# Kernel optimization log

Measured on AMD Instinct MI355X. Metric: run time of the kernel, lower is better.

## Reference

```python
import jax, jax.numpy as jnp
import numpy as np

NE, NR, D, H, L = 200000, 500, 128, 4, 2
HD = D // H
N, E, B = 32768, 262144, 256
MARGIN = 1.0


def setup_inputs() -> dict:
    key = jax.random.key(0)
    ks = jax.random.split(key, 16)
    nrm = lambda k, shp, s=0.05: jax.random.normal(k, shp, jnp.float32) * s
    inp = {
        'ent_emb': nrm(ks[0], (NE, D)),
        'rel_emb': nrm(ks[1], (NR, D)),
        'rel_prior': nrm(ks[2], (NR, 1)),
    }
    for i, nm in enumerate(['Wq', 'Wk', 'Wv', 'Wo', 'Wek', 'Wev']):
        inp[nm] = nrm(ks[3 + i], (L, D, D))
    for gi, g in enumerate(['h', 't', 'n']):
        kb = jax.random.fold_in(key, 100 + gi)
        k1, k2, k3, k4 = jax.random.split(kb, 4)
        inp[f'x_{g}'] = jax.random.randint(k1, (N,), 0, NE, jnp.int32)
        inp[f'ei_{g}'] = jax.random.randint(k2, (2, E), 0, N, jnp.int32)
        inp[f'ea_{g}'] = jax.random.randint(k3, (E,), 0, NR, jnp.int32)
        inp[f'y_{g}'] = jax.random.randint(k4, (B,), 0, N // B, jnp.int32)
        inp[f's_{g}'] = jnp.full((B,), N // B, dtype=jnp.int32)
    inp['sample'] = jax.random.randint(ks[9], (B, 3), 0, NR, jnp.int32)
    return inp


def gnn_embed(ent_emb, rel_emb, rel_prior, Wq, Wk, Wv, Wo, Wek, Wev, x, ei, ea, y, s):
    n = x.shape[0]
    h = ent_emb[x]                    # [N, D] node features (embedding lookup)
    e_emb = rel_emb[ea]               # [E, D] edge relation embedding
    e_pri = rel_prior[ea]             # [E, 1] scalar relation prior gate
    src, dst = ei[0], ei[1]
    scale = 1.0 / np.sqrt(HD).astype(np.float32)
    for l in range(L):
        q = (h @ Wq[l]).reshape(n, H, HD)[dst]                               # [E,H,HD]
        k = (h @ Wk[l]).reshape(n, H, HD)[src] + (e_emb @ Wek[l]).reshape(-1, H, HD)
        v = (h @ Wv[l]).reshape(n, H, HD)[src] + (e_emb @ Wev[l]).reshape(-1, H, HD)
        score = jnp.sum(q * k, axis=-1) * scale * e_pri                      # [E,H]
        # segment softmax over incoming edges of each destination node
        m = jax.ops.segment_max(score, dst, num_segments=n)
        m = jnp.where(jnp.isfinite(m), m, 0.0)
        ex = jnp.exp(score - m[dst])
        den = jax.ops.segment_sum(ex, dst, num_segments=n)[dst]
        alpha = ex / (den + 1e-16)                                           # [E,H]
        msg = jax.ops.segment_sum((alpha[..., None] * v).reshape(-1, D), dst, num_segments=n)
        h = jax.nn.gelu(h + msg @ Wo[l])                                     # residual + activation
    # get_real_index: exclusive cumsum of graph sizes + local target index
    offsets = jnp.concatenate([jnp.zeros((1,), s.dtype), jnp.cumsum(s)[:-1]])
    return h[offsets + y]             # [B, D]


def reference(ent_emb, rel_emb, rel_prior, Wq, Wk, Wv, Wo, Wek, Wev,
              x_h, ei_h, ea_h, y_h, s_h,
              x_t, ei_t, ea_t, y_t, s_t,
              x_n, ei_n, ea_n, y_n, s_n, sample):
    g = lambda x, ei, ea, y, s: gnn_embed(ent_emb, rel_emb, rel_prior, Wq, Wk, Wv, Wo, Wek, Wev, x, ei, ea, y, s)
    h = g(x_h, ei_h, ea_h, y_h, s_h)[:, None, :]   # [B,1,D]
    t = g(x_t, ei_t, ea_t, y_t, s_t)[:, None, :]
    tn = g(x_n, ei_n, ea_n, y_n, s_n)[:, None, :]
    r = rel_emb[sample[:, 1]][:, None, :]          # [B,1,D]
    proj_t = h + r                                 # TransE projection
    pos = jnp.linalg.norm(t - proj_t + 1e-8, axis=2)   # [B,1]
    negs = jnp.linalg.norm(t - tn + 1e-8, axis=2)      # [B,1]
    neg = jnp.mean(negs, axis=-1)                      # [B]
    # MarginRankingLoss(pos, neg, target=-1): mean(max(0, (pos-neg)+margin)); broadcasts [B,1]-[B] -> [B,B]
    loss = jnp.mean(jnp.maximum(pos - neg + MARGIN, 0.0))
    return loss
```

## Files before the change

### kernel.cpp

```cpp
#include <hip/hip_runtime.h>
#include <hip/hip_bf16.h>
#include <math.h>

#define NEC 200000
#define NRC 500
#define DD 128
#define LLC 2
#define NNODE 32768
#define EEDGE 262144
#define BBATCH 256
#define NG 3
#define BCAP 32

typedef __attribute__((ext_vector_type(8))) short short8;
typedef __attribute__((ext_vector_type(4))) float floatx4;
typedef __attribute__((ext_vector_type(2))) float floatx2;

__device__ __forceinline__ float bf2f(unsigned short u) {
  union { unsigned int i; float f; } c; c.i = ((unsigned int)u) << 16; return c.f;
}
__device__ __forceinline__ unsigned short f2bf(float f) {
  union { float f; unsigned int i; } c; c.f = f;
  unsigned int x = c.i;
  unsigned int r = x + 0x7fffu + ((x >> 16) & 1u);
  return (unsigned short)(r >> 16);
}
__device__ __forceinline__ float bfu_lo(unsigned int u) {
  union { unsigned int i; float f; } c; c.i = u << 16; return c.f;
}
__device__ __forceinline__ float bfu_hi(unsigned int u) {
  union { unsigned int i; float f; } c; c.i = u & 0xffff0000u; return c.f;
}

__device__ __forceinline__ bool detect_fm(const void* ent) {
  unsigned int u = ((const unsigned int*)ent)[threadIdx.x & 63];
  bool big = fabsf(bfu_lo(u)) > 100.f;
  return __ballot(big) != 0ull;
}

__global__ __launch_bounds__(128) void k_prep(const void* ent, const void* rel,
    const void* prior, const void* Wq, const void* Wk, const void* Wv, const void* Wo,
    const void* Wek, const void* Wev,
    float* pris, unsigned short* WT, unsigned short* relk, unsigned short* relv, int* deg) {
  bool fm = detect_fm(ent);
  int bid = blockIdx.x, tid = threadIdx.x;
  if (bid < 4) {
    int r = bid * 128 + tid;
    if (r < NRC) {
      float p = fm ? ((const float*)prior)[r] : bf2f(((const unsigned short*)prior)[r]);
      pris[r] = p * 0.17677669529663687f;
    }
  } else if (bid < 1028) {
    int t = (bid - 4) * 128 + tid;
    int mat = t >> 15;
    int rem = t & 32767;
    int l = rem >> 14;
    int p = rem & 16383;
    int d = p >> 7, c = p & 127;
    const void* W = mat == 0 ? Wq : (mat == 1 ? Wk : (mat == 2 ? Wv : Wo));
    size_t src = (size_t)l * DD * DD + (size_t)c * DD + d;
    float v = fm ? ((const float*)W)[src] : bf2f(((const unsigned short*)W)[src]);
    WT[(((size_t)mat * LLC + l) * DD + d) * DD + c] = f2bf(v);
  } else if (bid < 3028) {
    int rid = bid - 1028;
    int which = rid / 1000;
    int l = (rid / 500) % 2;
    int r = rid % 500;
    int d = tid;
    size_t wofs = (size_t)l * DD * DD;
    const float* Wf = (const float*)(which ? Wev : Wek) + wofs;
    const unsigned short* Wb = (const unsigned short*)(which ? Wev : Wek) + wofs;
    __shared__ float re[DD];
    re[d] = fm ? ((const float*)rel)[r * DD + d] : bf2f(((const unsigned short*)rel)[r * DD + d]);
    __syncthreads();
    float acc = 0.f;
    if (fm) { for (int c = 0; c < DD; ++c) acc += re[c] * Wf[c * DD + d]; }
    else    { for (int c = 0; c < DD; ++c) acc += re[c] * bf2f(Wb[c * DD + d]); }
    unsigned short* out = which ? relv : relk;
    out[((size_t)l * NRC + r) * DD + d] = f2bf(acc);
  } else {
    int t = (bid - 3028) * 128 + tid;
    uint4 z = {0u, 0u, 0u, 0u};
    ((uint4*)deg)[t * 2] = z;
    ((uint4*)deg)[t * 2 + 1] = z;
  }
}

__global__ __launch_bounds__(256) void k_gb(const void* ent,
    const int* x0, const int* x1, const int* x2,
    const int* ei0, const int* ea0, const int* ei1, const int* ea1,
    const int* ei2, const int* ea2,
    unsigned short* hbf, int* deg, unsigned int* bucket) {
  int bid = blockIdx.x, tid = threadIdx.x;
  if (bid < 3072) {
    bool fm = detect_fm(ent);
    int rbase = bid * 32;
    int g = rbase >> 15;
    const int* x = g == 0 ? x0 : (g == 1 ? x1 : x2);
    int c = tid & 31;
    int j4 = tid >> 5;
    int rows[4], xs[4];
    #pragma unroll
    for (int k = 0; k < 4; ++k) {
      rows[k] = rbase + j4 + 8 * k;
      xs[k] = x[rows[k] & (NNODE - 1)];
    }
    if (fm) {
      float4 v[4];
      #pragma unroll
      for (int k = 0; k < 4; ++k)
        v[k] = *reinterpret_cast<const float4*>((const float*)ent + (size_t)xs[k] * DD + c * 4);
      #pragma unroll
      for (int k = 0; k < 4; ++k) {
        uint2 o;
        o.x = ((unsigned int)f2bf(v[k].y) << 16) | (unsigned int)f2bf(v[k].x);
        o.y = ((unsigned int)f2bf(v[k].w) << 16) | (unsigned int)f2bf(v[k].z);
        *reinterpret_cast<uint2*>(hbf + (size_t)rows[k] * DD + c * 4) = o;
      }
    } else {
      uint2 v[4];
      #pragma unroll
      for (int k = 0; k < 4; ++k)
        v[k] = *reinterpret_cast<const uint2*>((const unsigned short*)ent + (size_t)xs[k] * DD + c * 4);
      #pragma unroll
      for (int k = 0; k < 4; ++k)
        *reinterpret_cast<uint2*>(hbf + (size_t)rows[k] * DD + c * 4) = v[k];
    }
  } else {
    int bb = bid - 3072;
    int g = bb >> 10;
    const int* ei = g == 0 ? ei0 : (g == 1 ? ei1 : ei2);
    const int* ea = g == 0 ? ea0 : (g == 1 ? ea1 : ea2);
    int e = (bb & 1023) * 256 + tid;
    int dst = ei[EEDGE + e];
    int src = ei[e];
    int r = ea[e];
    int pos = atomicAdd(&deg[g * NNODE + dst], 1);
    if (pos < BCAP)
      bucket[((size_t)g * NNODE + dst) * BCAP + pos] = (unsigned int)src | ((unsigned int)r << 15);
  }
}

__device__ __forceinline__ void stage_wt(const unsigned short* WT, int tid,
                                         unsigned short (*Wt)[136]) {
  #pragma unroll
  for (int pass = 0; pass < 8; ++pass) {
    int idx = pass * 256 + tid;
    int d = idx >> 4, c0 = (idx & 15) << 3;
    *reinterpret_cast<short8*>(&Wt[d][c0]) =
        *reinterpret_cast<const short8*>(WT + d * DD + c0);
  }
}

__global__ __launch_bounds__(256) void k_gemm_qkv(const unsigned short* A,
    const unsigned short* WT, int layer, unsigned short* Qo, unsigned char* KV) {
  __shared__ unsigned short Wt[DD][136];
  int mat = blockIdx.y;
  int g = blockIdx.z;
  const unsigned short* Ag = A + (size_t)g * NNODE * DD;
  int tid = threadIdx.x;
  stage_wt(WT + ((size_t)mat * LLC + layer) * DD * DD, tid, Wt);
  __syncthreads();
  int w = tid >> 6, lane = tid & 63;
  int m = lane & 15, quad = lane >> 4;
  int row = blockIdx.x * 64 + w * 16 + m;
  floatx4 acc[8];
  #pragma unroll
  for (int t = 0; t < 8; ++t) acc[t] = (floatx4){0.f, 0.f, 0.f, 0.f};
  const unsigned short* arow = Ag + (size_t)row * DD;
  #pragma unroll
  for (int ks = 0; ks < 4; ++ks) {
    short8 a = *reinterpret_cast<const short8*>(arow + ks * 32 + quad * 8);
    #pragma unroll
    for (int t = 0; t < 8; ++t) {
      short8 b = *reinterpret_cast<const short8*>(&Wt[t * 16 + m][ks * 32 + quad * 8]);
      acc[t] = __builtin_amdgcn_mfma_f32_16x16x32_bf16(a, b, acc[t], 0, 0, 0);
    }
  }
  __syncthreads();
  unsigned short* ut = &Wt[0][0];
  #pragma unroll
  for (int t = 0; t < 8; ++t) {
    #pragma unroll
    for (int r = 0; r < 4; ++r) {
      ut[(w * 16 + quad * 4 + r) * 136 + t * 16 + m] = f2bf(acc[t][r]);
    }
  }
  __syncthreads();
  int rowbase = blockIdx.x * 64;
  if (mat == 0) {
    unsigned short* Og = Qo + (size_t)g * NNODE * DD;
    #pragma unroll
    for (int k = 0; k < 4; ++k) {
      int flat = k * 256 + tid;
      int rw = flat >> 4, c8 = flat & 15;
      short8 v = *reinterpret_cast<const short8*>(ut + rw * 136 + c8 * 8);
      *reinterpret_cast<short8*>(Og + (size_t)(rowbase + rw) * DD + c8 * 8) = v;
    }
  } else {
    unsigned char* kvb = KV + (size_t)g * NNODE * 256 + (mat == 1 ? 0 : 128);
    #pragma unroll
    for (int k = 0; k < 2; ++k) {
      int flat = k * 256 + tid;
      int rw = flat >> 3, c16 = flat & 7;
      const unsigned short* p = ut + rw * 136 + c16 * 16;
      uint4 a = *reinterpret_cast<const uint4*>(p);
      uint4 b = *reinterpret_cast<const uint4*>(p + 8);
      unsigned int w0 = __builtin_amdgcn_cvt_pk_fp8_f32(bfu_lo(a.x), bfu_hi(a.x), 0u, false);
      w0 = __builtin_amdgcn_cvt_pk_fp8_f32(bfu_lo(a.y), bfu_hi(a.y), w0, true);
      unsigned int w1 = __builtin_amdgcn_cvt_pk_fp8_f32(bfu_lo(a.z), bfu_hi(a.z), 0u, false);
      w1 = __builtin_amdgcn_cvt_pk_fp8_f32(bfu_lo(a.w), bfu_hi(a.w), w1, true);
      unsigned int w2 = __builtin_amdgcn_cvt_pk_fp8_f32(bfu_lo(b.x), bfu_hi(b.x), 0u, false);
      w2 = __builtin_amdgcn_cvt_pk_fp8_f32(bfu_lo(b.y), bfu_hi(b.y), w2, true);
      unsigned int w3 = __builtin_amdgcn_cvt_pk_fp8_f32(bfu_lo(b.z), bfu_hi(b.z), 0u, false);
      w3 = __builtin_amdgcn_cvt_pk_fp8_f32(bfu_lo(b.w), bfu_hi(b.w), w3, true);
      uint4 o = {w0, w1, w2, w3};
      *reinterpret_cast<uint4*>(kvb + (size_t)(rowbase + rw) * 256 + c16 * 16) = o;
    }
  }
}

__global__ __launch_bounds__(256) void k_gemm_o(const unsigned short* A,
    const unsigned short* WT, int layer, unsigned short* hbf) {
  __shared__ unsigned short Wt[DD][136];
  int g = blockIdx.y;
  const unsigned short* Ag = A + (size_t)g * NNODE * DD;
  unsigned short* hbg = hbf + (size_t)g * NNODE * DD;
  int tid = threadIdx.x;
  stage_wt(WT + ((size_t)3 * LLC + layer) * DD * DD, tid, Wt);
  __syncthreads();
  int w = tid >> 6, lane = tid & 63;
  int m = lane & 15, quad = lane >> 4;
  int row = blockIdx.x * 64 + w * 16 + m;
  floatx4 acc[8];
  #pragma unroll
  for (int t = 0; t < 8; ++t) acc[t] = (floatx4){0.f, 0.f, 0.f, 0.f};
  const unsigned short* arow = Ag + (size_t)row * DD;
  #pragma unroll
  for (int ks = 0; ks < 4; ++ks) {
    short8 a = *reinterpret_cast<const short8*>(arow + ks * 32 + quad * 8);
    #pragma unroll
    for (int t = 0; t < 8; ++t) {
      short8 b = *reinterpret_cast<const short8*>(&Wt[t * 16 + m][ks * 32 + quad * 8]);
      acc[t] = __builtin_amdgcn_mfma_f32_16x16x32_bf16(a, b, acc[t], 0, 0, 0);
    }
  }
  __syncthreads();
  float* ft = (float*)&Wt[0][0];
  #pragma unroll
  for (int t = 0; t < 8; ++t) {
    #pragma unroll
    for (int r = 0; r < 4; ++r) {
      ft[(w * 16 + quad * 4 + r) * 136 + t * 16 + m] = acc[t][r];
    }
  }
  __syncthreads();
  int rowbase = blockIdx.x * 64;
  #pragma unroll
  for (int k = 0; k < 8; ++k) {
    int flat = k * 256 + tid;
    int rw = flat >> 5, c4 = flat & 31;
    float4 v = *reinterpret_cast<const float4*>(ft + rw * 136 + c4 * 4);
    size_t gi = (size_t)(rowbase + rw) * DD + c4 * 4;
    uint2 hv = *reinterpret_cast<const uint2*>(hbg + gi);
    float h0 = bfu_lo(hv.x), h1 = bfu_hi(hv.x), h2 = bfu_lo(hv.y), h3 = bfu_hi(hv.y);
    float r0, r1, r2, r3;
    {
      float xv = v.x + h0;
      float z2 = 1.5957691216057308f * (xv + 0.044715f * xv * xv * xv);
      r0 = xv / (1.f + __expf(-z2));
      xv = v.y + h1;
      z2 = 1.5957691216057308f * (xv + 0.044715f * xv * xv * xv);
      r1 = xv / (1.f + __expf(-z2));
      xv = v.z + h2;
      z2 = 1.5957691216057308f * (xv + 0.044715f * xv * xv * xv);
      r2 = xv / (1.f + __expf(-z2));
      xv = v.w + h3;
      z2 = 1.5957691216057308f * (xv + 0.044715f * xv * xv * xv);
      r3 = xv / (1.f + __expf(-z2));
    }
    uint2 o;
    o.x = ((unsigned int)f2bf(r1) << 16) | (unsigned int)f2bf(r0);
    o.y = ((unsigned int)f2bf(r3) << 16) | (unsigned int)f2bf(r2);
    *reinterpret_cast<uint2*>(hbg + gi) = o;
  }
}

__global__ __launch_bounds__(256) void k_attn(const unsigned short* Q, const unsigned char* KV,
    const unsigned short* relk, const unsigned short* relv,
    const float* pris, const int* deg, const unsigned int* bucket, int layer,
    unsigned short* msgb) {
  int w = threadIdx.x >> 6, lane = threadIdx.x & 63;
  int quarter = lane >> 4, sl = lane & 15;
  int g = blockIdx.y;
  int dst = blockIdx.x * 4 + w;
  const unsigned short* rk = relk + (size_t)layer * NRC * DD;
  const unsigned short* rv = relv + (size_t)layer * NRC * DD;
  const unsigned char* KVg = KV + (size_t)g * NNODE * 256;
  size_t gofs = (size_t)g * NNODE * DD;

  uint4 qu = *reinterpret_cast<const uint4*>(Q + gofs + (size_t)dst * DD + sl * 8);
  float q0 = bfu_lo(qu.x), q1 = bfu_hi(qu.x), q2 = bfu_lo(qu.y), q3 = bfu_hi(qu.y);
  float q4 = bfu_lo(qu.z), q5 = bfu_hi(qu.z), q6 = bfu_lo(qu.w), q7 = bfu_hi(qu.w);

  float den = 0.f;
  float m0 = 0.f, m1 = 0.f, m2 = 0.f, m3 = 0.f, m4 = 0.f, m5 = 0.f, m6 = 0.f, m7 = 0.f;
  int dg = deg[g * NNODE + dst]; if (dg > BCAP) dg = BCAP;
  size_t base = ((size_t)g * NNODE + dst) * BCAP;
  if (dg > 0) {
    int niter = (dg + 3) >> 2;
    unsigned int pe = bucket[base + (quarter < dg ? quarter : dg - 1)];
    for (int i = 0; i < niter; ++i) {
      unsigned int cur = pe;
      int nx = 4 * (i + 1) + quarter; if (nx >= dg) nx = dg - 1;
      pe = bucket[base + nx];
      int src = (int)(cur & 32767u);
      int r = (int)(cur >> 15);
      const unsigned char* kvrow = KVg + (size_t)src * 256;
      uint2 k8 = *reinterpret_cast<const uint2*>(kvrow + sl * 8);
      uint2 v8 = *reinterpret_cast<const uint2*>(kvrow + 128 + sl * 8);
      uint4 rku = *reinterpret_cast<const uint4*>(rk + (size_t)r * DD + sl * 8);
      uint4 rvu = *reinterpret_cast<const uint4*>(rv + (size_t)r * DD + sl * 8);
      float p = pris[r];
      floatx2 k01 = __builtin_amdgcn_cvt_pk_f32_fp8(k8.x, false);
      floatx2 k23 = __builtin_amdgcn_cvt_pk_f32_fp8(k8.x, true);
      floatx2 k45 = __builtin_amdgcn_cvt_pk_f32_fp8(k8.y, false);
      floatx2 k67 = __builtin_amdgcn_cvt_pk_f32_fp8(k8.y, true);
      float s = q0 * (k01.x + bfu_lo(rku.x))
              + q1 * (k01.y + bfu_hi(rku.x))
              + q2 * (k23.x + bfu_lo(rku.y))
              + q3 * (k23.y + bfu_hi(rku.y))
              + q4 * (k45.x + bfu_lo(rku.z))
              + q5 * (k45.y + bfu_hi(rku.z))
              + q6 * (k67.x + bfu_lo(rku.w))
              + q7 * (k67.y + bfu_hi(rku.w));
      s += __shfl_xor(s, 1); s += __shfl_xor(s, 2);
      bool valid = (4 * i + quarter) < dg;
      float ex = valid ? __expf(s * p) : 0.f;
      floatx2 v01 = __builtin_amdgcn_cvt_pk_f32_fp8(v8.x, false);
      floatx2 v23 = __builtin_amdgcn_cvt_pk_f32_fp8(v8.x, true);
      floatx2 v45 = __builtin_amdgcn_cvt_pk_f32_fp8(v8.y, false);
      floatx2 v67 = __builtin_amdgcn_cvt_pk_f32_fp8(v8.y, true);
      den += ex;
      m0 += ex * (v01.x + bfu_lo(rvu.x));
      m1 += ex * (v01.y + bfu_hi(rvu.x));
      m2 += ex * (v23.x + bfu_lo(rvu.y));
      m3 += ex * (v23.y + bfu_hi(rvu.y));
      m4 += ex * (v45.x + bfu_lo(rvu.z));
      m5 += ex * (v45.y + bfu_hi(rvu.z));
      m6 += ex * (v67.x + bfu_lo(rvu.w));
      m7 += ex * (v67.y + bfu_hi(rvu.w));
    }
  }
  den += __shfl_xor(den, 16); den += __shfl_xor(den, 32);
  m0 += __shfl_xor(m0, 16); m0 += __shfl_xor(m0, 32);
  m1 += __shfl_xor(m1, 16); m1 += __shfl_xor(m1, 32);
  m2 += __shfl_xor(m2, 16); m2 += __shfl_xor(m2, 32);
  m3 += __shfl_xor(m3, 16); m3 += __shfl_xor(m3, 32);
  m4 += __shfl_xor(m4, 16); m4 += __shfl_xor(m4, 32);
  m5 += __shfl_xor(m5, 16); m5 += __shfl_xor(m5, 32);
  m6 += __shfl_xor(m6, 16); m6 += __shfl_xor(m6, 32);
  m7 += __shfl_xor(m7, 16); m7 += __shfl_xor(m7, 32);
  float inv = 1.f / (den + 1e-16f);
  if (quarter == 0) {
    uint4 o;
    o.x = ((unsigned int)f2bf(m1 * inv) << 16) | (unsigned int)f2bf(m0 * inv);
    o.y = ((unsigned int)f2bf(m3 * inv) << 16) | (unsigned int)f2bf(m2 * inv);
    o.z = ((unsigned int)f2bf(m5 * inv) << 16) | (unsigned int)f2bf(m4 * inv);
    o.w = ((unsigned int)f2bf(m7 * inv) << 16) | (unsigned int)f2bf(m6 * inv);
    *reinterpret_cast<uint4*>(msgb + gofs + (size_t)dst * DD + sl * 8) = o;
  }
}

__global__ __launch_bounds__(128) void k_ep(const unsigned short* hbf, const void* ent,
    const void* rel,
    const int* y0, const int* s0, const int* y1, const int* s1, const int* y2, const int* s2,
    const int* sample, float* pos, float* neg) {
  bool fm = detect_fm(ent);
  int b = blockIdx.x, d = threadIdx.x;
  int oh = 0, ot = 0, on = 0;
  for (int j = 0; j < b; ++j) { oh += s0[j]; ot += s1[j]; on += s2[j]; }
  int ih = oh + y0[b], it = ot + y1[b], in_ = on + y2[b];
  float th = bf2f(hbf[((size_t)0 * NNODE + ih) * DD + d]);
  float tt = bf2f(hbf[((size_t)1 * NNODE + it) * DD + d]);
  float tn = bf2f(hbf[((size_t)2 * NNODE + in_) * DD + d]);
  int r = sample[b * 3 + 1];
  float rr = fm ? ((const float*)rel)[r * DD + d] : bf2f(((const unsigned short*)rel)[r * DD + d]);
  float dp = tt - (th + rr) + 1e-8f;
  float dn = tt - tn + 1e-8f;
  float ap = dp * dp, an = dn * dn;
  for (int o = 32; o > 0; o >>= 1) { ap += __shfl_down(ap, o); an += __shfl_down(an, o); }
  __shared__ float sa[2], sb[2];
  if ((d & 63) == 0) { sa[d >> 6] = ap; sb[d >> 6] = an; }
  __syncthreads();
  if (d == 0) { pos[b] = sqrtf(sa[0] + sa[1]); neg[b] = sqrtf(sb[0] + sb[1]); }
}

__global__ __launch_bounds__(256) void k_hinge(const float* pos, const float* neg,
    const void* ent, void* out) {
  bool fm = detect_fm(ent);
  __shared__ float ns[BBATCH];
  __shared__ float wsum[4];
  int t = threadIdx.x;
  ns[t] = neg[t];
  float pb = pos[t];
  __syncthreads();
  float local = 0.f;
  for (int j = 0; j < BBATCH; ++j) {
    float v = pb - ns[j] + 1.0f;
    local += v > 0.f ? v : 0.f;
  }
  for (int o = 32; o > 0; o >>= 1) local += __shfl_down(local, o);
  if ((t & 63) == 0) wsum[t >> 6] = local;
  __syncthreads();
  if (t == 0) {
    float loss = (wsum[0] + wsum[1] + wsum[2] + wsum[3]) * (1.f / (256.f * 256.f));
    if (fm) ((float*)out)[0] = loss;
    else    ((unsigned short*)out)[0] = f2bf(loss);
  }
}

extern "C" void kernel_launch(void* const* d_in, const int* in_sizes, int n_in,
                              void* d_out, int out_size, void* d_ws, size_t ws_size,
                              hipStream_t stream) {
  const void* ent   = d_in[0];
  const void* rel   = d_in[1];
  const void* prior = d_in[2];
  const void* Wq  = d_in[3];
  const void* Wk  = d_in[4];
  const void* Wv  = d_in[5];
  const void* Wo  = d_in[6];
  const void* Wek = d_in[7];
  const void* Wev = d_in[8];
  const int* sample = (const int*)d_in[24];

  size_t off = 0;
  char* basep = (char*)d_ws;
  auto alloc = [&](size_t bytes) -> void* {
    void* r = basep + off;
    off = (off + bytes + 255) & ~(size_t)255;
    return r;
  };
  unsigned short* hbf  = (unsigned short*)alloc((size_t)NG * NNODE * DD * 2);
  unsigned short* Qb   = (unsigned short*)alloc((size_t)NG * NNODE * DD * 2);
  unsigned char*  KV   = (unsigned char*)alloc((size_t)NG * NNODE * 256);
  unsigned short* msgb = (unsigned short*)alloc((size_t)NG * NNODE * DD * 2);
  unsigned short* relk = (unsigned short*)alloc((size_t)LLC * NRC * DD * 2);
  unsigned short* relv = (unsigned short*)alloc((size_t)LLC * NRC * DD * 2);
  unsigned short* WT   = (unsigned short*)alloc((size_t)4 * LLC * DD * DD * 2);
  float* pris = (float*)alloc((size_t)NRC * 4);
  int*   deg  = (int*)alloc((size_t)NG * NNODE * 4);
  unsigned int* bucket = (unsigned int*)alloc((size_t)NG * NNODE * BCAP * 4);
  float* pos  = (float*)alloc((size_t)BBATCH * 4);
  float* neg  = (float*)alloc((size_t)BBATCH * 4);

  const int* x0  = (const int*)d_in[9],  *x1 = (const int*)d_in[14], *x2 = (const int*)d_in[19];
  const int* ei0 = (const int*)d_in[10], *ei1 = (const int*)d_in[15], *ei2 = (const int*)d_in[20];
  const int* ea0 = (const int*)d_in[11], *ea1 = (const int*)d_in[16], *ea2 = (const int*)d_in[21];
  const int* y0  = (const int*)d_in[12], *y1 = (const int*)d_in[17], *y2 = (const int*)d_in[22];
  const int* s0  = (const int*)d_in[13], *s1 = (const int*)d_in[18], *s2 = (const int*)d_in[23];

  k_prep<<<3124, 128, 0, stream>>>(ent, rel, prior, Wq, Wk, Wv, Wo, Wek, Wev,
                                   pris, WT, relk, relv, deg);
  k_gb<<<6144, 256, 0, stream>>>(ent, x0, x1, x2, ei0, ea0, ei1, ea1, ei2, ea2,
                                 hbf, deg, bucket);
  for (int l = 0; l < LLC; ++l) {
    k_gemm_qkv<<<dim3(NNODE / 64, 3, NG), 256, 0, stream>>>(hbf, WT, l, Qb, KV);
    k_attn<<<dim3(NNODE / 4, NG), 256, 0, stream>>>(Qb, KV, relk, relv, pris, deg, bucket, l, msgb);
    k_gemm_o<<<dim3(NNODE / 64, NG), 256, 0, stream>>>(msgb, WT, l, hbf);
  }
  k_ep<<<BBATCH, 128, 0, stream>>>(hbf, ent, rel, y0, s0, y1, s1, y2, s2, sample, pos, neg);
  k_hinge<<<1, BBATCH, 0, stream>>>(pos, neg, ent, d_out);
}
```

Before: 487.1 us.

## Process two destinations per wave in attention and vectorize edge bucketing

The attention kernel now assigns two destination nodes per 64-lane wave: each half-wave of 32 lanes handles one node, with two edges in flight per iteration instead of four. This cuts wasted lanes, since average in-degree is about 8, and halves the cross-lane reduction. The edge-bucketing part of the build kernel loads four edges per thread with 128-bit loads, so it needs fewer blocks. Each node's edge loop is now longer, which adds serial latency per wave.

```diff
diff --git a/kernel.cpp b/kernel.cpp
--- a/kernel.cpp
+++ b/kernel.cpp
@@ -128,16 +128,24 @@
     }
   } else {
     int bb = bid - 3072;
-    int g = bb >> 10;
+    int g = bb >> 8;
     const int* ei = g == 0 ? ei0 : (g == 1 ? ei1 : ei2);
     const int* ea = g == 0 ? ea0 : (g == 1 ? ea1 : ea2);
-    int e = (bb & 1023) * 256 + tid;
-    int dst = ei[EEDGE + e];
-    int src = ei[e];
-    int r = ea[e];
-    int pos = atomicAdd(&deg[g * NNODE + dst], 1);
-    if (pos < BCAP)
-      bucket[((size_t)g * NNODE + dst) * BCAP + pos] = (unsigned int)src | ((unsigned int)r << 15);
+    int e0 = (bb & 255) * 1024 + tid * 4;
+    uint4 d4 = *reinterpret_cast<const uint4*>(ei + EEDGE + e0);
+    uint4 s4 = *reinterpret_cast<const uint4*>(ei + e0);
+    uint4 r4 = *reinterpret_cast<const uint4*>(ea + e0);
+    int* degg = deg + g * NNODE;
+    size_t brow = (size_t)g * NNODE;
+    #pragma unroll
+    for (int k = 0; k < 4; ++k) {
+      int dst = (int)((const unsigned int*)&d4)[k];
+      unsigned int src = ((const unsigned int*)&s4)[k];
+      unsigned int r = ((const unsigned int*)&r4)[k];
+      int pos = atomicAdd(&degg[dst], 1);
+      if (pos < BCAP)
+        bucket[(brow + dst) * BCAP + pos] = src | (r << 15);
+    }
   }
 }
 
@@ -291,9 +299,11 @@
     const float* pris, const int* deg, const unsigned int* bucket, int layer,
     unsigned short* msgb) {
   int w = threadIdx.x >> 6, lane = threadIdx.x & 63;
-  int quarter = lane >> 4, sl = lane & 15;
+  int half = lane >> 5;
+  int hq = (lane >> 4) & 1;
+  int sl = lane & 15;
   int g = blockIdx.y;
-  int dst = blockIdx.x * 4 + w;
+  int dst = blockIdx.x * 8 + w * 2 + half;
   const unsigned short* rk = relk + (size_t)layer * NRC * DD;
   const unsigned short* rv = relv + (size_t)layer * NRC * DD;
   const unsigned char* KVg = KV + (size_t)g * NNODE * 256;
@@ -308,11 +318,11 @@
   int dg = deg[g * NNODE + dst]; if (dg > BCAP) dg = BCAP;
   size_t base = ((size_t)g * NNODE + dst) * BCAP;
   if (dg > 0) {
-    int niter = (dg + 3) >> 2;
-    unsigned int pe = bucket[base + (quarter < dg ? quarter : dg - 1)];
+    int niter = (dg + 1) >> 1;
+    unsigned int pe = bucket[base + (hq < dg ? hq : dg - 1)];
     for (int i = 0; i < niter; ++i) {
       unsigned int cur = pe;
-      int nx = 4 * (i + 1) + quarter; if (nx >= dg) nx = dg - 1;
+      int nx = 2 * (i + 1) + hq; if (nx >= dg) nx = dg - 1;
       pe = bucket[base + nx];
       int src = (int)(cur & 32767u);
       int r = (int)(cur >> 15);
@@ -335,7 +345,7 @@
               + q6 * (k67.x + bfu_lo(rku.w))
               + q7 * (k67.y + bfu_hi(rku.w));
       s += __shfl_xor(s, 1); s += __shfl_xor(s, 2);
-      bool valid = (4 * i + quarter) < dg;
+      bool valid = (2 * i + hq) < dg;
       float ex = valid ? __expf(s * p) : 0.f;
       floatx2 v01 = __builtin_amdgcn_cvt_pk_f32_fp8(v8.x, false);
       floatx2 v23 = __builtin_amdgcn_cvt_pk_f32_fp8(v8.x, true);
@@ -352,17 +362,17 @@
       m7 += ex * (v67.y + bfu_hi(rvu.w));
     }
   }
-  den += __shfl_xor(den, 16); den += __shfl_xor(den, 32);
-  m0 += __shfl_xor(m0, 16); m0 += __shfl_xor(m0, 32);
-  m1 += __shfl_xor(m1, 16); m1 += __shfl_xor(m1, 32);
-  m2 += __shfl_xor(m2, 16); m2 += __shfl_xor(m2, 32);
-  m3 += __shfl_xor(m3, 16); m3 += __shfl_xor(m3, 32);
-  m4 += __shfl_xor(m4, 16); m4 += __shfl_xor(m4, 32);
-  m5 += __shfl_xor(m5, 16); m5 += __shfl_xor(m5, 32);
-  m6 += __shfl_xor(m6, 16); m6 += __shfl_xor(m6, 32);
-  m7 += __shfl_xor(m7, 16); m7 += __shfl_xor(m7, 32);
+  den += __shfl_xor(den, 16);
+  m0 += __shfl_xor(m0, 16);
+  m1 += __shfl_xor(m1, 16);
+  m2 += __shfl_xor(m2, 16);
+  m3 += __shfl_xor(m3, 16);
+  m4 += __shfl_xor(m4, 16);
+  m5 += __shfl_xor(m5, 16);
+  m6 += __shfl_xor(m6, 16);
+  m7 += __shfl_xor(m7, 16);
   float inv = 1.f / (den + 1e-16f);
-  if (quarter == 0) {
+  if (hq == 0) {
     uint4 o;
     o.x = ((unsigned int)f2bf(m1 * inv) << 16) | (unsigned int)f2bf(m0 * inv);
     o.y = ((unsigned int)f2bf(m3 * inv) << 16) | (unsigned int)f2bf(m2 * inv);
@@ -462,11 +472,11 @@
 
   k_prep<<<3124, 128, 0, stream>>>(ent, rel, prior, Wq, Wk, Wv, Wo, Wek, Wev,
                                    pris, WT, relk, relv, deg);
-  k_gb<<<6144, 256, 0, stream>>>(ent, x0, x1, x2, ei0, ea0, ei1, ea1, ei2, ea2,
+  k_gb<<<3840, 256, 0, stream>>>(ent, x0, x1, x2, ei0, ea0, ei1, ea1, ei2, ea2,
                                  hbf, deg, bucket);
   for (int l = 0; l < LLC; ++l) {
     k_gemm_qkv<<<dim3(NNODE / 64, 3, NG), 256, 0, stream>>>(hbf, WT, l, Qb, KV);
-    k_attn<<<dim3(NNODE / 4, NG), 256, 0, stream>>>(Qb, KV, relk, relv, pris, deg, bucket, l, msgb);
+    k_attn<<<dim3(NNODE / 8, NG), 256, 0, stream>>>(Qb, KV, relk, relv, pris, deg, bucket, l, msgb);
     k_gemm_o<<<dim3(NNODE / 64, NG), 256, 0, stream>>>(msgb, WT, l, hbf);
   }
   k_ep<<<BBATCH, 128, 0, stream>>>(hbf, ent, rel, y0, s0, y1, s1, y2, s2, sample, pos, neg);
```

Result: faster. 477.5 us (-2.0%).
